# Optimization experiments

Hardware: AMD Instinct MI355X
Metric: run time of the kernel (lower is better)

## Reference

```python
import jax, jax.numpy as jnp
import numpy as np

C1 = 512  # channels1 (query input dim)
C = 512   # channels (model dim)


def setup_inputs() -> dict:
    key = jax.random.key(0)
    ks = jax.random.split(key, 12)
    B, Lq, Lk = 8, 2048, 2048
    s1 = 1.0 / np.sqrt(C1)
    s = 1.0 / np.sqrt(C)
    return {
        "rep": jax.random.normal(ks[0], (B, Lq, C1), dtype=jnp.float32),
        "rep1": jax.random.normal(ks[1], (B, Lk, C), dtype=jnp.float32),
        "Wq_w": jax.random.uniform(ks[2], (C1, C), jnp.float32, -s1, s1),
        "Wq_b": jax.random.uniform(ks[3], (C,), jnp.float32, -s1, s1),
        "Wk_w": jax.random.uniform(ks[4], (C, C), jnp.float32, -s, s),
        "Wk_b": jax.random.uniform(ks[5], (C,), jnp.float32, -s, s),
        "Wv_w": jax.random.uniform(ks[6], (C, C), jnp.float32, -s, s),
        "Wv_b": jax.random.uniform(ks[7], (C,), jnp.float32, -s, s),
        "FC_w": jax.random.uniform(ks[8], (C, C), jnp.float32, -s, s),
        "FC_b": jax.random.uniform(ks[9], (C,), jnp.float32, -s, s),
    }


def reference(rep, rep1, Wq_w, Wq_b, Wk_w, Wk_b, Wv_w, Wv_b, FC_w, FC_b):
    # Linear + ReLU projections (single head)
    q = jax.nn.relu(jnp.einsum('blc,cd->bld', rep, Wq_w) + Wq_b)    # [B,Lq,C]
    k = jax.nn.relu(jnp.einsum('blc,cd->bld', rep1, Wk_w) + Wk_b)   # [B,Lk,C]
    v = jax.nn.relu(jnp.einsum('blc,cd->bld', rep1, Wv_w) + Wv_b)   # [B,Lk,C]
    scores = jnp.einsum('bqd,bkd->bqk', q, k) / jnp.sqrt(jnp.float32(C))
    attn = jax.nn.softmax(scores, axis=-1)                           # [B,Lq,Lk]
    out = jnp.einsum('bqk,bkd->bqd', attn, v)                        # [B,Lq,C]
    out = jax.nn.relu(jnp.einsum('bld,de->ble', out, FC_w) + FC_b)
    return out
```

## Files before the change

### kernel.cpp

```cpp
#include <hip/hip_runtime.h>


typedef __attribute__((ext_vector_type(8))) short short8;
typedef __attribute__((ext_vector_type(4))) float f32x4;

#define SEQ 2048
#define CH 512
#define NB 8
#define MTOT (NB * SEQ)

#define GLDS16(gp, lp)                                                                  \
  __builtin_amdgcn_global_load_lds((const __attribute__((address_space(1))) void*)(gp), \
                                   (__attribute__((address_space(3))) void*)(lp), 16, 0, 0)

__device__ __forceinline__ unsigned short f2bf(float f) {
  unsigned u = __float_as_uint(f);
  u += 0x7fffu + ((u >> 16) & 1u);
  return (unsigned short)(u >> 16);
}

__global__ void cvt_bf16_kernel(const float* __restrict__ in0, unsigned short* __restrict__ out0,
                                const float* __restrict__ in1, unsigned short* __restrict__ out1) {
  int blk = blockIdx.x;
  const float* in = (blk < 4096) ? in0 : in1;
  unsigned short* out = (blk < 4096) ? out0 : out1;
  blk &= 4095;
  long i = ((long)blk * 256 + threadIdx.x) * 8;
  float4 a = *(const float4*)(in + i);
  float4 b = *(const float4*)(in + i + 4);
  ushort4 o0, o1;
  o0.x = f2bf(a.x); o0.y = f2bf(a.y); o0.z = f2bf(a.z); o0.w = f2bf(a.w);
  o1.x = f2bf(b.x); o1.y = f2bf(b.y); o1.z = f2bf(b.z); o1.w = f2bf(b.w);
  *(ushort4*)(out + i) = o0;
  *(ushort4*)(out + i + 4) = o1;
}

__global__ __launch_bounds__(256) void wtrans_kernel(const float* __restrict__ W0,
                                                     const float* __restrict__ W1,
                                                     const float* __restrict__ W2,
                                                     const float* __restrict__ W3,
                                                     unsigned short* __restrict__ Wt) {
  __shared__ __attribute__((aligned(16))) unsigned short tile[64 * 72];
  const int z = blockIdx.z;
  const float* W = (z == 0) ? W0 : (z == 1) ? W1 : (z == 2) ? W2 : W3;
  unsigned short* Wtz = Wt + (long)z * 512 * 512;
  const int t = threadIdx.x;
  const int k0 = blockIdx.y * 64, n0 = blockIdx.x * 64;
  const int r = t >> 4, cq = (t & 15) * 4;
#pragma unroll
  for (int j = 0; j < 4; ++j) {
    int row = r + 16 * j;
    float4 v = *(const float4*)&W[(long)(k0 + row) * 512 + n0 + cq];
    tile[row * 72 + cq + 0] = f2bf(v.x);
    tile[row * 72 + cq + 1] = f2bf(v.y);
    tile[row * 72 + cq + 2] = f2bf(v.z);
    tile[row * 72 + cq + 3] = f2bf(v.w);
  }
  __syncthreads();
#pragma unroll
  for (int j = 0; j < 4; ++j) {
    int row = r + 16 * j;
    ushort4 o;
    o.x = tile[(cq + 0) * 72 + row];
    o.y = tile[(cq + 1) * 72 + row];
    o.z = tile[(cq + 2) * 72 + row];
    o.w = tile[(cq + 3) * 72 + row];
    *(ushort4*)&Wtz[(long)(n0 + row) * 512 + k0 + cq] = o;
  }
}

__global__ __launch_bounds__(256) void vtrans_kernel(const unsigned short* __restrict__ V,
                                                     unsigned short* __restrict__ Vt) {
  __shared__ __attribute__((aligned(16))) unsigned short tile[64 * 72];
  const int t = threadIdx.x;
  const int b = blockIdx.z;
  const int kk0 = blockIdx.y * 64;
  const int d0 = blockIdx.x * 64;
  const unsigned short* Vb = V + (long)b * SEQ * CH;
  unsigned short* Vtb = Vt + (long)b * CH * SEQ;
  const int r = t >> 4, cq = (t & 15) * 4;
#pragma unroll
  for (int j = 0; j < 4; ++j) {
    int row = r + 16 * j;
    ushort4 v = *(const ushort4*)&Vb[(long)(kk0 + row) * CH + d0 + cq];
    tile[row * 72 + cq + 0] = v.x;
    tile[row * 72 + cq + 1] = v.y;
    tile[row * 72 + cq + 2] = v.z;
    tile[row * 72 + cq + 3] = v.w;
  }
  __syncthreads();
#pragma unroll
  for (int j = 0; j < 4; ++j) {
    int row = r + 16 * j;
    ushort4 o;
    o.x = tile[(cq + 0) * 72 + row];
    o.y = tile[(cq + 1) * 72 + row];
    o.z = tile[(cq + 2) * 72 + row];
    o.w = tile[(cq + 3) * 72 + row];
    *(ushort4*)&Vtb[(long)(d0 + row) * SEQ + kk0 + cq] = o;
  }
}

template <int EPI, int LDA, int LDB, int LDO, int K>
__global__ __launch_bounds__(256) void gemm_nt(const unsigned short* __restrict__ A, long sAb,
                                               const unsigned short* __restrict__ Bt, long sBb,
                                               const float* __restrict__ bias,
                                               float* __restrict__ rowsum, long sRb,
                                               void* __restrict__ outp, long sOb) {
  __shared__ __attribute__((aligned(16))) unsigned short Al[128 * 32];
  __shared__ __attribute__((aligned(16))) unsigned short Bl[128 * 32];
  const int t = threadIdx.x;
  const int w = t >> 6, l = t & 63;
  const int wr = w >> 1, wc = w & 1;
  const int lr = l & 15, lg = l >> 4, lc = lg * 8;
  const int bz = blockIdx.z;
  const long m0 = (long)blockIdx.y * 128, n0 = (long)blockIdx.x * 128;
  const int srow = 32 * w + (l >> 2);
  const int scol = (l & 3) * 8;
  const unsigned short* ga = A + bz * sAb + (long)(m0 + srow) * LDA + scol;
  const unsigned short* gb = Bt + bz * sBb + (long)(n0 + srow) * LDB + scol;
  unsigned short* la = &Al[(32 * w) * 32];
  unsigned short* lb = &Bl[(32 * w) * 32];

  f32x4 acc[4][4] = {};
  for (int k0 = 0; k0 < K; k0 += 32) {
    GLDS16(ga, la);
    GLDS16(ga + 16 * LDA, la + 16 * 32);
    GLDS16(gb, lb);
    GLDS16(gb + 16 * LDB, lb + 16 * 32);
    ga += 32; gb += 32;
    __syncthreads();
    short8 af[4], bfr[4];
#pragma unroll
    for (int i = 0; i < 4; ++i) {
      af[i]  = *(short8*)&Al[(64 * wr + 16 * i + lr) * 32 + lc];
      bfr[i] = *(short8*)&Bl[(64 * wc + 16 * i + lr) * 32 + lc];
    }
#pragma unroll
    for (int mi = 0; mi < 4; ++mi)
#pragma unroll
      for (int ni = 0; ni < 4; ++ni)
        acc[mi][ni] = __builtin_amdgcn_mfma_f32_16x16x32_bf16(af[mi], bfr[ni], acc[mi][ni], 0, 0, 0);
    __syncthreads();
  }

  if (EPI == 0 || EPI == 1) {
    float bv[4];
#pragma unroll
    for (int ni = 0; ni < 4; ++ni) bv[ni] = bias[n0 + 64 * wc + 16 * ni + lr];
#pragma unroll
    for (int mi = 0; mi < 4; ++mi)
#pragma unroll
      for (int ni = 0; ni < 4; ++ni)
#pragma unroll
        for (int r = 0; r < 4; ++r) {
          long row = m0 + 64 * wr + 16 * mi + lg * 4 + r;
          long col = n0 + 64 * wc + 16 * ni + lr;
          float v = fmaxf(acc[mi][ni][r] + bv[ni], 0.0f);
          if (EPI == 1) ((unsigned short*)outp)[bz * sOb + row * LDO + col] = f2bf(v);
          else          ((float*)outp)[bz * sOb + row * LDO + col] = v;
        }
  } else if (EPI == 2) {
    unsigned short* P = (unsigned short*)outp + bz * sOb;
    float* rs = rowsum + bz * sRb;
    float rsum[4][4] = {};
#pragma unroll
    for (int mi = 0; mi < 4; ++mi)
#pragma unroll
      for (int ni = 0; ni < 4; ++ni)
#pragma unroll
        for (int r = 0; r < 4; ++r) {
          long row = m0 + 64 * wr + 16 * mi + lg * 4 + r;
          long col = n0 + 64 * wc + 16 * ni + lr;
          float p = exp2f(acc[mi][ni][r] * 0.06375872f);
          unsigned short pb = f2bf(p);
          P[row * LDO + col] = pb;
          rsum[mi][r] += __uint_as_float((unsigned)pb << 16);
        }
#pragma unroll
    for (int off = 1; off < 16; off <<= 1)
#pragma unroll
      for (int mi = 0; mi < 4; ++mi)
#pragma unroll
        for (int r = 0; r < 4; ++r) rsum[mi][r] += __shfl_xor(rsum[mi][r], off);
    if (lr == 0) {
#pragma unroll
      for (int mi = 0; mi < 4; ++mi)
#pragma unroll
        for (int r = 0; r < 4; ++r)
          atomicAdd(&rs[m0 + 64 * wr + 16 * mi + lg * 4 + r], rsum[mi][r]);
    }
  } else {
    unsigned short* O = (unsigned short*)outp + bz * sOb;
    const float* rs = rowsum + bz * sRb;
    float inv[4][4];
#pragma unroll
    for (int mi = 0; mi < 4; ++mi)
#pragma unroll
      for (int r = 0; r < 4; ++r)
        inv[mi][r] = 1.0f / rs[m0 + 64 * wr + 16 * mi + lg * 4 + r];
#pragma unroll
    for (int mi = 0; mi < 4; ++mi)
#pragma unroll
      for (int ni = 0; ni < 4; ++ni)
#pragma unroll
        for (int r = 0; r < 4; ++r) {
          long row = m0 + 64 * wr + 16 * mi + lg * 4 + r;
          long col = n0 + 64 * wc + 16 * ni + lr;
          O[row * LDO + col] = f2bf(acc[mi][ni][r] * inv[mi][r]);
        }
  }
}

extern "C" void kernel_launch(void* const* d_in, const int* in_sizes, int n_in,
                              void* d_out, int out_size, void* d_ws, size_t ws_size,
                              hipStream_t stream) {
  const float* rep  = (const float*)d_in[0];
  const float* rep1 = (const float*)d_in[1];
  const float* Wq_w = (const float*)d_in[2];
  const float* Wq_b = (const float*)d_in[3];
  const float* Wk_w = (const float*)d_in[4];
  const float* Wk_b = (const float*)d_in[5];
  const float* Wv_w = (const float*)d_in[6];
  const float* Wv_b = (const float*)d_in[7];
  const float* FC_w = (const float*)d_in[8];
  const float* FC_b = (const float*)d_in[9];
  float* out = (float*)d_out;
  char* ws = (char*)d_ws;

  const size_t SZB = (size_t)MTOT * CH * 2;
  const size_t SZP = (size_t)NB * SEQ * SEQ * 2;
  const size_t SZR = (size_t)MTOT * 4;
  const size_t need = 6 * SZB + 4 * (size_t)512 * 512 * 2 + SZP + SZR;
  if (ws_size < need) return;

  unsigned short* Qb    = (unsigned short*)(ws + 0 * SZB);
  unsigned short* Kbuf  = (unsigned short*)(ws + 1 * SZB);
  unsigned short* Vbuf  = (unsigned short*)(ws + 2 * SZB);
  unsigned short* Vtb   = (unsigned short*)(ws + 3 * SZB);
  unsigned short* repb  = (unsigned short*)(ws + 4 * SZB);
  unsigned short* rep1b = (unsigned short*)(ws + 5 * SZB);
  unsigned short* Wt4   = (unsigned short*)(ws + 6 * SZB);
  unsigned short* Wtq   = Wt4;
  unsigned short* Wtk   = Wtq + 512 * 512;
  unsigned short* Wtv   = Wtk + 512 * 512;
  unsigned short* Wtf   = Wtv + 512 * 512;
  unsigned short* Pbuf  = (unsigned short*)(ws + 6 * SZB + 4 * (size_t)512 * 512 * 2);
  float*          rowsum = (float*)((char*)Pbuf + SZP);

  hipMemsetAsync(rowsum, 0, SZR, stream);

  cvt_bf16_kernel<<<8192, 256, 0, stream>>>(rep, repb, rep1, rep1b);
  wtrans_kernel<<<dim3(8, 8, 4), 256, 0, stream>>>(Wq_w, Wk_w, Wv_w, FC_w, Wt4);

  gemm_nt<1, CH, CH, CH, CH><<<dim3(4, 128, 1), 256, 0, stream>>>(repb, 0, Wtq, 0, Wq_b,
                                                                  nullptr, 0, Qb, 0);
  gemm_nt<1, CH, CH, CH, CH><<<dim3(4, 128, 1), 256, 0, stream>>>(rep1b, 0, Wtk, 0, Wk_b,
                                                                  nullptr, 0, Kbuf, 0);
  gemm_nt<1, CH, CH, CH, CH><<<dim3(4, 128, 1), 256, 0, stream>>>(rep1b, 0, Wtv, 0, Wv_b,
                                                                  nullptr, 0, Vbuf, 0);

  vtrans_kernel<<<dim3(8, 32, 8), 256, 0, stream>>>(Vbuf, Vtb);

  gemm_nt<2, CH, CH, SEQ, CH><<<dim3(16, 16, 8), 256, 0, stream>>>(
      Qb, (long)SEQ * CH, Kbuf, (long)SEQ * CH, nullptr, rowsum, SEQ,
      Pbuf, (long)SEQ * SEQ);

  gemm_nt<3, SEQ, SEQ, CH, SEQ><<<dim3(4, 16, 8), 256, 0, stream>>>(
      Pbuf, (long)SEQ * SEQ, Vtb, (long)CH * SEQ, nullptr, rowsum, SEQ,
      Vbuf, (long)SEQ * CH);

  gemm_nt<0, CH, CH, CH, CH><<<dim3(4, 128, 1), 256, 0, stream>>>(Vbuf, 0, Wtf, 0, FC_b,
                                                                  nullptr, 0, out, 0);
}
```

Measured before the change: 324.7 us.

## Double K-tile depth, XOR-swizzle LDS, and stage epilogue stores through LDS

The GEMM K-step grows from 32 to 64, which halves the number of barrier pairs per tile. The LDS layout uses an XOR swizzle to avoid bank conflicts on the 64-wide rows. The epilogues now write each 16-row patch of the accumulator into LDS and read it back as vector rows, so global stores become coalesced 16-byte writes instead of scattered 2- or 4-byte writes. The costs are double the LDS footprint and extra barriers inside the epilogue.

```diff
diff --git a/kernel.cpp b/kernel.cpp
--- a/kernel.cpp
+++ b/kernel.cpp
@@ -107,108 +107,130 @@
                                                const float* __restrict__ bias,
                                                float* __restrict__ rowsum, long sRb,
                                                void* __restrict__ outp, long sOb) {
-  __shared__ __attribute__((aligned(16))) unsigned short Al[128 * 32];
-  __shared__ __attribute__((aligned(16))) unsigned short Bl[128 * 32];
+  __shared__ __attribute__((aligned(16))) unsigned short Al[128 * 64];
+  __shared__ __attribute__((aligned(16))) unsigned short Bl[128 * 64];
   const int t = threadIdx.x;
   const int w = t >> 6, l = t & 63;
   const int wr = w >> 1, wc = w & 1;
-  const int lr = l & 15, lg = l >> 4, lc = lg * 8;
+  const int lr = l & 15, lg = l >> 4;
   const int bz = blockIdx.z;
   const long m0 = (long)blockIdx.y * 128, n0 = (long)blockIdx.x * 128;
-  const int srow = 32 * w + (l >> 2);
-  const int scol = (l & 3) * 8;
-  const unsigned short* ga = A + bz * sAb + (long)(m0 + srow) * LDA + scol;
-  const unsigned short* gb = Bt + bz * sBb + (long)(n0 + srow) * LDB + scol;
-  unsigned short* la = &Al[(32 * w) * 32];
-  unsigned short* lb = &Bl[(32 * w) * 32];
+  const int srow = 32 * w + (l >> 3);
+  const int sxor = ((l & 7) ^ (l >> 3)) * 8;
+  const unsigned short* ga = A + bz * sAb + (long)(m0 + srow) * LDA + sxor;
+  const unsigned short* gb = Bt + bz * sBb + (long)(n0 + srow) * LDB + sxor;
+  unsigned short* la = &Al[32 * w * 64];
+  unsigned short* lb = &Bl[32 * w * 64];
 
   f32x4 acc[4][4] = {};
-  for (int k0 = 0; k0 < K; k0 += 32) {
-    GLDS16(ga, la);
-    GLDS16(ga + 16 * LDA, la + 16 * 32);
-    GLDS16(gb, lb);
-    GLDS16(gb + 16 * LDB, lb + 16 * 32);
-    ga += 32; gb += 32;
+  for (int k0 = 0; k0 < K; k0 += 64) {
+#pragma unroll
+    for (int j = 0; j < 4; ++j) {
+      GLDS16(ga + (long)8 * j * LDA, la + j * 512);
+      GLDS16(gb + (long)8 * j * LDB, lb + j * 512);
+    }
+    ga += 64; gb += 64;
     __syncthreads();
-    short8 af[4], bfr[4];
-#pragma unroll
-    for (int i = 0; i < 4; ++i) {
-      af[i]  = *(short8*)&Al[(64 * wr + 16 * i + lr) * 32 + lc];
-      bfr[i] = *(short8*)&Bl[(64 * wc + 16 * i + lr) * 32 + lc];
-    }
-#pragma unroll
-    for (int mi = 0; mi < 4; ++mi)
+#pragma unroll
+    for (int h = 0; h < 2; ++h) {
+      short8 af[4], bfr[4];
+#pragma unroll
+      for (int i = 0; i < 4; ++i) {
+        const int kc = ((h * 4 + lg) ^ (lr & 7)) * 8;
+        af[i]  = *(short8*)&Al[(64 * wr + 16 * i + lr) * 64 + kc];
+        bfr[i] = *(short8*)&Bl[(64 * wc + 16 * i + lr) * 64 + kc];
+      }
+#pragma unroll
+      for (int mi = 0; mi < 4; ++mi)
+#pragma unroll
+        for (int ni = 0; ni < 4; ++ni)
+          acc[mi][ni] =
+              __builtin_amdgcn_mfma_f32_16x16x32_bf16(af[mi], bfr[ni], acc[mi][ni], 0, 0, 0);
+    }
+    __syncthreads();
+  }
+
+  if (EPI == 0) {
+    float* patchF = (float*)(w < 2 ? Al : Bl) + (w & 1) * 1024;
+    float* O = (float*)outp + bz * sOb;
+    float bv[4];
+#pragma unroll
+    for (int ni = 0; ni < 4; ++ni) bv[ni] = bias[n0 + 64 * wc + 16 * ni + lr];
+#pragma unroll
+    for (int mi = 0; mi < 4; ++mi) {
+      const long rowb = m0 + 64 * wr + 16 * mi;
 #pragma unroll
       for (int ni = 0; ni < 4; ++ni)
-        acc[mi][ni] = __builtin_amdgcn_mfma_f32_16x16x32_bf16(af[mi], bfr[ni], acc[mi][ni], 0, 0, 0);
-    __syncthreads();
-  }
-
-  if (EPI == 0 || EPI == 1) {
+#pragma unroll
+        for (int r = 0; r < 4; ++r)
+          patchF[(lg * 4 + r) * 64 + 16 * ni + lr] = fmaxf(acc[mi][ni][r] + bv[ni], 0.0f);
+      __syncthreads();
+#pragma unroll
+      for (int j = 0; j < 4; ++j) {
+        float4 x = *(float4*)&patchF[(4 * j + (l >> 4)) * 64 + (l & 15) * 4];
+        *(float4*)&O[(rowb + 4 * j + (l >> 4)) * LDO + n0 + 64 * wc + (l & 15) * 4] = x;
+      }
+      __syncthreads();
+    }
+  } else {
+    unsigned short* patch = &Al[w * 16 * 72];
+    unsigned short* O = (unsigned short*)outp + bz * sOb;
     float bv[4];
-#pragma unroll
-    for (int ni = 0; ni < 4; ++ni) bv[ni] = bias[n0 + 64 * wc + 16 * ni + lr];
-#pragma unroll
-    for (int mi = 0; mi < 4; ++mi)
+    if (EPI == 1) {
+#pragma unroll
+      for (int ni = 0; ni < 4; ++ni) bv[ni] = bias[n0 + 64 * wc + 16 * ni + lr];
+    }
+    float rsum[4][4] = {};
+    const float* rsin = (EPI == 3) ? rowsum + bz * sRb : nullptr;
+#pragma unroll
+    for (int mi = 0; mi < 4; ++mi) {
+      const long rowb = m0 + 64 * wr + 16 * mi;
+      float invr[4];
+      if (EPI == 3) {
+#pragma unroll
+        for (int r = 0; r < 4; ++r) invr[r] = 1.0f / rsin[rowb + lg * 4 + r];
+      }
 #pragma unroll
       for (int ni = 0; ni < 4; ++ni)
 #pragma unroll
         for (int r = 0; r < 4; ++r) {
-          long row = m0 + 64 * wr + 16 * mi + lg * 4 + r;
-          long col = n0 + 64 * wc + 16 * ni + lr;
-          float v = fmaxf(acc[mi][ni][r] + bv[ni], 0.0f);
-          if (EPI == 1) ((unsigned short*)outp)[bz * sOb + row * LDO + col] = f2bf(v);
-          else          ((float*)outp)[bz * sOb + row * LDO + col] = v;
+          float a = acc[mi][ni][r];
+          unsigned short ob;
+          if (EPI == 1) {
+            ob = f2bf(fmaxf(a + bv[ni], 0.0f));
+          } else if (EPI == 2) {
+            float p = exp2f(a * 0.06375872f);
+            ob = f2bf(p);
+            rsum[mi][r] += __uint_as_float((unsigned)ob << 16);
+          } else {
+            ob = f2bf(a * invr[r]);
+          }
+          patch[(lg * 4 + r) * 72 + 16 * ni + lr] = ob;
         }
-  } else if (EPI == 2) {
-    unsigned short* P = (unsigned short*)outp + bz * sOb;
-    float* rs = rowsum + bz * sRb;
-    float rsum[4][4] = {};
-#pragma unroll
-    for (int mi = 0; mi < 4; ++mi)
-#pragma unroll
-      for (int ni = 0; ni < 4; ++ni)
-#pragma unroll
-        for (int r = 0; r < 4; ++r) {
-          long row = m0 + 64 * wr + 16 * mi + lg * 4 + r;
-          long col = n0 + 64 * wc + 16 * ni + lr;
-          float p = exp2f(acc[mi][ni][r] * 0.06375872f);
-          unsigned short pb = f2bf(p);
-          P[row * LDO + col] = pb;
-          rsum[mi][r] += __uint_as_float((unsigned)pb << 16);
-        }
-#pragma unroll
-    for (int off = 1; off < 16; off <<= 1)
-#pragma unroll
-      for (int mi = 0; mi < 4; ++mi)
-#pragma unroll
-        for (int r = 0; r < 4; ++r) rsum[mi][r] += __shfl_xor(rsum[mi][r], off);
-    if (lr == 0) {
-#pragma unroll
-      for (int mi = 0; mi < 4; ++mi)
-#pragma unroll
-        for (int r = 0; r < 4; ++r)
-          atomicAdd(&rs[m0 + 64 * wr + 16 * mi + lg * 4 + r], rsum[mi][r]);
-    }
-  } else {
-    unsigned short* O = (unsigned short*)outp + bz * sOb;
-    const float* rs = rowsum + bz * sRb;
-    float inv[4][4];
-#pragma unroll
-    for (int mi = 0; mi < 4; ++mi)
-#pragma unroll
-      for (int r = 0; r < 4; ++r)
-        inv[mi][r] = 1.0f / rs[m0 + 64 * wr + 16 * mi + lg * 4 + r];
-#pragma unroll
-    for (int mi = 0; mi < 4; ++mi)
-#pragma unroll
-      for (int ni = 0; ni < 4; ++ni)
-#pragma unroll
-        for (int r = 0; r < 4; ++r) {
-          long row = m0 + 64 * wr + 16 * mi + lg * 4 + r;
-          long col = n0 + 64 * wc + 16 * ni + lr;
-          O[row * LDO + col] = f2bf(acc[mi][ni][r] * inv[mi][r]);
-        }
+      __syncthreads();
+#pragma unroll
+      for (int j = 0; j < 2; ++j) {
+        short8 x = *(short8*)&patch[(l >> 2) * 72 + j * 32 + (l & 3) * 8];
+        *(short8*)&O[(rowb + (l >> 2)) * LDO + n0 + 64 * wc + j * 32 + (l & 3) * 8] = x;
+      }
+      __syncthreads();
+    }
+    if (EPI == 2) {
+      float* rs = rowsum + bz * sRb;
+#pragma unroll
+      for (int off = 1; off < 16; off <<= 1)
+#pragma unroll
+        for (int mi = 0; mi < 4; ++mi)
+#pragma unroll
+          for (int r = 0; r < 4; ++r) rsum[mi][r] += __shfl_xor(rsum[mi][r], off);
+      if (lr == 0) {
+#pragma unroll
+        for (int mi = 0; mi < 4; ++mi)
+#pragma unroll
+          for (int r = 0; r < 4; ++r)
+            atomicAdd(&rs[m0 + 64 * wr + 16 * mi + lg * 4 + r], rsum[mi][r]);
+      }
+    }
   }
 }
 
```

Result: faster. 317.7 us (-2.2%).
